# Performance work log

Measured on AMD Instinct MI355X. Metric: run time of the kernel, lower is better.

The kernel has to match this reference:

```python
import jax, jax.numpy as jnp
import numpy as np

N = 50000   # team_count (num nodes)
E = 800000  # num edges
D = 64      # embed_dim
C = 32      # conv_out_channels
K = 3       # Chebyshev order
B = 16384   # number of games (len(home))


def setup_inputs() -> dict:
    key = jax.random.key(0)
    ks = jax.random.split(key, 20)
    inp = {
        "edge_index": jax.random.randint(ks[0], (2, E), 0, N),
        "home": jax.random.randint(ks[1], (B,), 0, N),
        "away": jax.random.randint(ks[2], (B,), 0, N),
        "edge_weight": jax.random.uniform(ks[3], (E,), dtype=jnp.float32),
        "embedding": jax.random.normal(ks[4], (N, D), dtype=jnp.float32) * 0.1,
    }
    def W(k, i, o):
        return jax.random.normal(k, (K, i, o), dtype=jnp.float32) * 0.05
    inp["Wxz"] = W(ks[5], D, C); inp["Whz"] = W(ks[6], C, C)
    inp["Wxr"] = W(ks[7], D, C); inp["Whr"] = W(ks[8], C, C)
    inp["Wxh"] = W(ks[9], D, C); inp["Whh"] = W(ks[10], C, C)
    for i, name in enumerate(["bxz", "bhz", "bxr", "bhr", "bxh", "bhh"]):
        inp[name] = jax.random.normal(ks[11 + i], (C,), dtype=jnp.float32) * 0.01
    return inp


def _cheb(x, W, b, row, col, w_hat, n):
    """PyG ChebConv with sym normalization, lambda_max=2: L_hat = -D^-1/2 A D^-1/2."""
    def prop(t):  # L_hat @ t  via gather->scale->scatter over edges
        return jax.ops.segment_sum(w_hat[:, None] * t[row], col, num_segments=n)
    Tx0 = x
    out = Tx0 @ W[0]
    Tx1 = prop(Tx0)
    out = out + Tx1 @ W[1]
    for k in range(2, W.shape[0]):
        Tx2 = 2.0 * prop(Tx1) - Tx0
        out = out + Tx2 @ W[k]
        Tx0, Tx1 = Tx1, Tx2
    return out + b


def reference(edge_index, home, away, edge_weight, embedding,
              Wxz, Whz, Wxr, Whr, Wxh, Whh,
              bxz, bhz, bxr, bhr, bxh, bhh):
    row, col = edge_index[0], edge_index[1]
    n = embedding.shape[0]
    deg = jax.ops.segment_sum(edge_weight, row, num_segments=n)
    dinv = jnp.where(deg > 0, jax.lax.rsqrt(deg), 0.0)
    w_hat = -dinv[row] * edge_weight * dinv[col]

    x = embedding                       # [N, D]
    H = jnp.zeros((n, Wxz.shape[-1]), x.dtype)  # initial hidden state
    cheb = lambda t, W, b: _cheb(t, W, b, row, col, w_hat, n)

    Z = jax.nn.sigmoid(cheb(x, Wxz, bxz) + cheb(H, Whz, bhz))
    R = jax.nn.sigmoid(cheb(x, Wxr, bxr) + cheb(H, Whr, bhr))
    H_tilde = jnp.tanh(cheb(x, Wxh, bxh) + cheb(H * R, Whh, bhh))
    H = Z * H + (1.0 - Z) * H_tilde     # [N, C]

    h = jnp.concatenate([H[home], H[away]], axis=0)  # [2B, C]
    return jax.nn.softmax(h, axis=0)    # torch Softmax(dim=0)
```

## Files before the change

kernel.cpp:

```cpp
#include <hip/hip_runtime.h>
#include <hip/hip_fp16.h>
#include <math.h>

constexpr int N_   = 50000;
constexpr int E_   = 800000;
constexpr int D_   = 64;
constexpr int C_   = 32;
constexpr int B_   = 16384;
constexpr int TWOB = 2 * B_;
constexpr int NB_SM = 256;
constexpr int NBINS = (N_ + 255) / 256;
constexpr int EPB   = 4096;
constexpr int NCH   = (E_ + EPB - 1) / EPB;
constexpr int CAPBB = 64;
constexpr int CAPB  = 5120;
constexpr int GN  = 64;
constexpr int LDP = 68;
constexpr int NPAD = 50176;

__device__ inline float4 ld_h4(const ushort* p) {
    uint2 u = *reinterpret_cast<const uint2*>(p);
    __half2 h0 = *reinterpret_cast<__half2*>(&u.x);
    __half2 h1 = *reinterpret_cast<__half2*>(&u.y);
    float2 f0 = __half22float2(h0), f1 = __half22float2(h1);
    return make_float4(f0.x, f0.y, f1.x, f1.y);
}
__device__ inline void st_h4(ushort* p, float4 v) {
    __half2 h0 = __floats2half2_rn(v.x, v.y);
    __half2 h1 = __floats2half2_rn(v.z, v.w);
    uint2 u;
    u.x = *reinterpret_cast<unsigned*>(&h0);
    u.y = *reinterpret_cast<unsigned*>(&h1);
    *reinterpret_cast<uint2*>(p) = u;
}

__device__ inline void excl_scan256(int* sc, int t, int c0, int* st) {
    sc[t] = c0;
    __syncthreads();
#pragma unroll
    for (int off = 1; off < 256; off <<= 1) {
        int v = (t >= off) ? sc[t - off] : 0;
        __syncthreads();
        sc[t] += v;
        __syncthreads();
    }
    st[t] = sc[t] - c0;
}

__global__ __launch_bounds__(256) void k_bin(const int* __restrict__ row,
                                             const int* __restrict__ col,
                                             const float* __restrict__ ew,
                                             int* __restrict__ colCnt,
                                             int* __restrict__ rowCnt,
                                             int2* __restrict__ colBins2,
                                             int2* __restrict__ rowBins2) {
    __shared__ int cnt[256], st[256], cur[256], sc[256];
    __shared__ int2 buf[EPB];
    int t = threadIdx.x, blk = blockIdx.x;
    int base = blk * EPB;
    int nE = min(EPB, E_ - base);

    cnt[t] = 0;
    __syncthreads();
    for (int i = t; i < nE; i += 256) atomicAdd(&cnt[col[base + i] >> 8], 1);
    __syncthreads();
    int c0 = cnt[t];
    excl_scan256(sc, t, c0, st);
    cur[t] = 0;
    __syncthreads();
    for (int i = t; i < nE; i += 256) {
        int c = col[base + i], r = row[base + i];
        float w = ew[base + i];
        int p = st[c >> 8] + atomicAdd(&cur[c >> 8], 1);
        buf[p] = make_int2((c << 16) | r, __float_as_int(w));
    }
    __syncthreads();
    for (int i = t; i < nE; i += 256) {
        int2 e = buf[i];
        int bin = (int)(((unsigned)e.x) >> 24);
        int local = i - st[bin];
        if (local < CAPBB) colBins2[((size_t)bin * NCH + blk) * CAPBB + local] = e;
    }
    colCnt[blk * 256 + t] = min(c0, CAPBB);
    __syncthreads();

    cnt[t] = 0;
    __syncthreads();
    for (int i = t; i < nE; i += 256) atomicAdd(&cnt[row[base + i] >> 8], 1);
    __syncthreads();
    c0 = cnt[t];
    excl_scan256(sc, t, c0, st);
    cur[t] = 0;
    __syncthreads();
    for (int i = t; i < nE; i += 256) {
        int r = row[base + i];
        float w = ew[base + i];
        int p = st[r >> 8] + atomicAdd(&cur[r >> 8], 1);
        buf[p] = make_int2(r, __float_as_int(w));
    }
    __syncthreads();
    for (int i = t; i < nE; i += 256) {
        int2 e = buf[i];
        int bin = (int)(((unsigned)e.x) >> 8);
        int local = i - st[bin];
        if (local < CAPBB) rowBins2[((size_t)bin * NCH + blk) * CAPBB + local] = e;
    }
    rowCnt[blk * 256 + t] = min(c0, CAPBB);
}

__global__ __launch_bounds__(256) void k_deg(const int* __restrict__ rowCnt,
                                             const int2* __restrict__ rowBins2,
                                             float* __restrict__ dinv) {
    __shared__ float acc[256];
    int t = threadIdx.x, b = blockIdx.x;
    acc[t] = 0.f;
    __syncthreads();
    if (t < NCH) {
        int n = rowCnt[t * 256 + b];
        const int2* ch = rowBins2 + ((size_t)b * NCH + t) * CAPBB;
        for (int i = 0; i < n; ++i) {
            int2 e = ch[i];
            atomicAdd(&acc[e.x & 255], __int_as_float(e.y));
        }
    }
    __syncthreads();
    int r = b * 256 + t;
    if (r < N_) {
        float d = acc[t];
        dinv[r] = (d > 0.f) ? 1.f / sqrtf(d) : 0.f;
    }
}

__global__ __launch_bounds__(256) void k_sort(const int* __restrict__ colCnt,
                                              const int2* __restrict__ colBins2,
                                              const float* __restrict__ dinv,
                                              int2* __restrict__ edges,
                                              int2* __restrict__ percol,
                                              float* __restrict__ colsum) {
    __shared__ int cnt[256], st[256], cur[256], sc[256], pref[256];
    __shared__ int2 sbuf[CAPB];
    int t = threadIdx.x, b = blockIdx.x;
    if (b == 0 && t < 64) colsum[t] = 0.f;
    int myc = (t < NCH) ? colCnt[t * 256 + b] : 0;
    excl_scan256(sc, t, myc, pref);
    cnt[t] = 0;
    __syncthreads();
    if (t < NCH) {
        const int2* ch = colBins2 + ((size_t)b * NCH + t) * CAPBB;
        int p0 = pref[t];
        for (int i = 0; i < myc; ++i) {
            if (p0 + i < CAPB) {
                int2 e = ch[i];
                sbuf[p0 + i] = e;
                atomicAdd(&cnt[(((unsigned)e.x) >> 16) & 255], 1);
            }
        }
    }
    __syncthreads();
    int nb = min(sc[255], CAPB);
    int c0 = cnt[t];
    __syncthreads();
    excl_scan256(sc, t, c0, st);
    cur[t] = 0;
    __syncthreads();
    for (int i = t; i < nb; i += 256) {
        int2 e = sbuf[i];
        unsigned m = (unsigned)e.x;
        int r = (int)(m & 0xffffu);
        int c = (int)(m >> 16);
        float w = -__int_as_float(e.y) * dinv[r] * dinv[c];
        int clow = c & 255;
        int p = st[clow] + atomicAdd(&cur[clow], 1);
        edges[b * CAPB + p] = make_int2(r, __float_as_int(w));
    }
    percol[b * 256 + t] = make_int2(b * CAPB + st[t], cnt[t]);
}

__global__ __launch_bounds__(256) void k_prop1(const int2* __restrict__ percol,
                                               const int2* __restrict__ edges,
                                               const float* __restrict__ x,
                                               ushort* __restrict__ tx1h) {
    int node = (blockIdx.x * 256 + threadIdx.x) >> 6;
    if (node >= N_) return;
    int lane = threadIdx.x & 63;
    int eslot = lane >> 4;
    int f4 = (lane & 15) << 2;
    int2 oc = percol[node];
    int beg = oc.x, n = oc.y;
    float4 acc = {0.f, 0.f, 0.f, 0.f};
    for (int cb = 0; cb < n; cb += 16) {
        int2 er = edges[beg + cb + (lane & 15)];
        int   rr = er.x;
        float wr = __int_as_float(er.y);
#pragma unroll
        for (int k = 0; k < 4; ++k) {
            int idx = cb + 4 * k + eslot;
            int   r = __shfl(rr, 4 * k + eslot, 64);
            float w = __shfl(wr, 4 * k + eslot, 64);
            bool ok = idx < n;
            int  rs = ok ? r : 0;
            float wm = ok ? w : 0.f;
            float4 v = *reinterpret_cast<const float4*>(x + (size_t)rs * D_ + f4);
            acc.x += wm * v.x;
            acc.y += wm * v.y;
            acc.z += wm * v.z;
            acc.w += wm * v.w;
        }
    }
    acc.x += __shfl_xor(acc.x, 16, 64); acc.y += __shfl_xor(acc.y, 16, 64);
    acc.z += __shfl_xor(acc.z, 16, 64); acc.w += __shfl_xor(acc.w, 16, 64);
    acc.x += __shfl_xor(acc.x, 32, 64); acc.y += __shfl_xor(acc.y, 32, 64);
    acc.z += __shfl_xor(acc.z, 32, 64); acc.w += __shfl_xor(acc.w, 32, 64);
    if (eslot == 0) st_h4(tx1h + (size_t)node * D_ + f4, acc);
}

__global__ __launch_bounds__(256) void k_prop2(const int2* __restrict__ percol,
                                               const int2* __restrict__ edges,
                                               const ushort* __restrict__ tx1h,
                                               const float* __restrict__ x,
                                               ushort* __restrict__ tx2h) {
    int node = (blockIdx.x * 256 + threadIdx.x) >> 6;
    if (node >= N_) return;
    int lane = threadIdx.x & 63;
    int eslot = lane >> 4;
    int f4 = (lane & 15) << 2;
    int2 oc = percol[node];
    int beg = oc.x, n = oc.y;
    float4 acc = {0.f, 0.f, 0.f, 0.f};
    for (int cb = 0; cb < n; cb += 16) {
        int2 er = edges[beg + cb + (lane & 15)];
        int   rr = er.x;
        float wr = __int_as_float(er.y);
#pragma unroll
        for (int k = 0; k < 4; ++k) {
            int idx = cb + 4 * k + eslot;
            int   r = __shfl(rr, 4 * k + eslot, 64);
            float w = __shfl(wr, 4 * k + eslot, 64);
            bool ok = idx < n;
            int  rs = ok ? r : 0;
            float wm = ok ? w : 0.f;
            float4 v = ld_h4(tx1h + (size_t)rs * D_ + f4);
            acc.x += wm * v.x;
            acc.y += wm * v.y;
            acc.z += wm * v.z;
            acc.w += wm * v.w;
        }
    }
    acc.x += __shfl_xor(acc.x, 16, 64); acc.y += __shfl_xor(acc.y, 16, 64);
    acc.z += __shfl_xor(acc.z, 16, 64); acc.w += __shfl_xor(acc.w, 16, 64);
    acc.x += __shfl_xor(acc.x, 32, 64); acc.y += __shfl_xor(acc.y, 32, 64);
    acc.z += __shfl_xor(acc.z, 32, 64); acc.w += __shfl_xor(acc.w, 32, 64);
    if (eslot == 0) {
        float4 xv = *reinterpret_cast<const float4*>(x + (size_t)node * D_ + f4);
        float4 o = {2.f * acc.x - xv.x, 2.f * acc.y - xv.y,
                    2.f * acc.z - xv.z, 2.f * acc.w - xv.w};
        st_h4(tx2h + (size_t)node * D_ + f4, o);
    }
}

__global__ __launch_bounds__(256) void k_gates(const float* __restrict__ x,
                                               const ushort* __restrict__ tx1h,
                                               const ushort* __restrict__ tx2h,
                                               const float* __restrict__ Wxz,
                                               const float* __restrict__ Wxh,
                                               const float* __restrict__ bxz,
                                               const float* __restrict__ bhz,
                                               const float* __restrict__ bxh,
                                               const float* __restrict__ bhh,
                                               float* __restrict__ H) {
    __shared__ float lA[GN * LDP];
    __shared__ float lB[D_ * LDP];
    int t = threadIdx.x;
    int node0 = blockIdx.x * GN;
    int valid = min(GN, N_ - node0);
    int tn = t >> 4, tc = t & 15;
    float acc[4][4] = {};
    for (int ch = 0; ch < 3; ++ch) {
        if (ch == 0) {
            const float* s = x + (size_t)node0 * D_;
#pragma unroll
            for (int j = 0; j < 4; ++j) {
                int q = t * 4 + j * 1024;
                int nd = q >> 6, dd = q & 63;
                float4 v = {0.f, 0.f, 0.f, 0.f};
                if (nd < valid) v = *reinterpret_cast<const float4*>(s + q);
                *reinterpret_cast<float4*>(&lA[nd * LDP + dd]) = v;
            }
        } else {
            const ushort* s = ((ch == 1) ? tx1h : tx2h) + (size_t)node0 * D_;
#pragma unroll
            for (int j = 0; j < 4; ++j) {
                int q = t * 4 + j * 1024;
                int nd = q >> 6, dd = q & 63;
                float4 v = {0.f, 0.f, 0.f, 0.f};
                if (nd < valid) v = ld_h4(s + q);
                *reinterpret_cast<float4*>(&lA[nd * LDP + dd]) = v;
            }
        }
#pragma unroll
        for (int j = 0; j < 4; ++j) {
            int q = t * 4 + j * 1024;
            int dd = q >> 6, jj = q & 63;
            const float* wsrc = (jj < 32) ? (Wxz + ch * 2048 + dd * 32 + jj)
                                          : (Wxh + ch * 2048 + dd * 32 + (jj - 32));
            *reinterpret_cast<float4*>(&lB[dd * LDP + jj]) =
                *reinterpret_cast<const float4*>(wsrc);
        }
        __syncthreads();
#pragma unroll 4
        for (int k0 = 0; k0 < D_; k0 += 4) {
            float4 a[4], b[4];
#pragma unroll
            for (int i = 0; i < 4; ++i)
                a[i] = *reinterpret_cast<const float4*>(&lA[(tn * 4 + i) * LDP + k0]);
#pragma unroll
            for (int kk = 0; kk < 4; ++kk)
                b[kk] = *reinterpret_cast<const float4*>(&lB[(k0 + kk) * LDP + tc * 4]);
#pragma unroll
            for (int i = 0; i < 4; ++i) {
                acc[i][0] += a[i].x * b[0].x + a[i].y * b[1].x + a[i].z * b[2].x + a[i].w * b[3].x;
                acc[i][1] += a[i].x * b[0].y + a[i].y * b[1].y + a[i].z * b[2].y + a[i].w * b[3].y;
                acc[i][2] += a[i].x * b[0].z + a[i].y * b[1].z + a[i].z * b[2].z + a[i].w * b[3].z;
                acc[i][3] += a[i].x * b[0].w + a[i].y * b[1].w + a[i].z * b[2].w + a[i].w * b[3].w;
            }
        }
        __syncthreads();
    }
#pragma unroll
    for (int i = 0; i < 4; ++i) {
        float4 v = {acc[i][0], acc[i][1], acc[i][2], acc[i][3]};
        *reinterpret_cast<float4*>(&lA[(tn * 4 + i) * LDP + tc * 4]) = v;
    }
    __syncthreads();
#pragma unroll
    for (int m = 0; m < 8; ++m) {
        int idx = t + m * 256;
        int nd = idx >> 5, c = idx & 31;
        if (nd < valid) {
            float az = lA[nd * LDP + c]       + bxz[c] + bhz[c];
            float ah = lA[nd * LDP + 32 + c]  + bxh[c] + bhh[c];
            float z  = 1.f / (1.f + expf(-az));
            H[(size_t)(node0 + nd) * C_ + c] = (1.f - z) * tanhf(ah);
        }
    }
}

__global__ __launch_bounds__(256) void k_gexpsum2(const int* __restrict__ home,
                                                  const int* __restrict__ away,
                                                  const float* __restrict__ H,
                                                  float* __restrict__ hbuf,
                                                  float* __restrict__ colsum) {
    __shared__ float sm[8][32];
    int c = threadIdx.x & 31, g = threadIdx.x >> 5;
    float s = 0.f;
    for (int r0 = blockIdx.x * 8; r0 < TWOB; r0 += gridDim.x * 8) {
        int r = r0 + g;
        int node = (r < B_) ? home[r] : away[r - B_];
        float e = expf(H[(size_t)node * C_ + c]);
        hbuf[(size_t)r * C_ + c] = e;
        s += e;
    }
    sm[g][c] = s;
    __syncthreads();
    if (g < 4) sm[g][c] += sm[g + 4][c];
    __syncthreads();
    if (g < 2) sm[g][c] += sm[g + 2][c];
    __syncthreads();
    if (g == 0) atomicAdd(&colsum[c], sm[0][c] + sm[1][c]);
}

__global__ __launch_bounds__(256) void k_norm(const float* __restrict__ hbuf,
                                              const float* __restrict__ colsum,
                                              float* __restrict__ out) {
    int i = blockIdx.x * 256 + threadIdx.x;
    if (i < TWOB * C_ / 4) {
        float4 v = reinterpret_cast<const float4*>(hbuf)[i];
        int c0 = (i * 4) & 31;
        float4 s = *reinterpret_cast<const float4*>(colsum + c0);
        float4 o;
        o.x = v.x / s.x;
        o.y = v.y / s.y;
        o.z = v.z / s.z;
        o.w = v.w / s.w;
        reinterpret_cast<float4*>(out)[i] = o;
    }
}

extern "C" void kernel_launch(void* const* d_in, const int* in_sizes, int n_in,
                              void* d_out, int out_size, void* d_ws, size_t ws_size,
                              hipStream_t stream) {
    const int*   edge_index = (const int*)d_in[0];
    const int*   row  = edge_index;
    const int*   col  = edge_index + E_;
    const int*   home = (const int*)d_in[1];
    const int*   away = (const int*)d_in[2];
    const float* ew   = (const float*)d_in[3];
    const float* x    = (const float*)d_in[4];
    const float* Wxz  = (const float*)d_in[5];
    const float* Wxh  = (const float*)d_in[9];
    const float* bxz  = (const float*)d_in[11];
    const float* bhz  = (const float*)d_in[12];
    const float* bxh  = (const float*)d_in[15];
    const float* bhh  = (const float*)d_in[16];
    float* out = (float*)d_out;
    float* ws = (float*)d_ws;

    const size_t o_colCnt  = 0;
    const size_t o_rowCnt  = o_colCnt + (size_t)NCH * 256;
    const size_t o_colsum  = o_rowCnt + (size_t)NCH * 256;
    const size_t o_dinv    = o_colsum + 64;
    const size_t o_colBins2 = o_dinv + NPAD;
    const size_t o_rowBins2 = o_colBins2 + 2 * (size_t)NBINS * NCH * CAPBB;
    const size_t o_edges   = o_rowBins2 + 2 * (size_t)NBINS * NCH * CAPBB;
    const size_t o_percol  = o_edges + 2 * (size_t)NBINS * CAPB + 32;
    const size_t o_tx1h    = o_percol + 2 * (size_t)NBINS * 256;
    const size_t o_tx2h    = o_tx1h + (size_t)N_ * D_ / 2;
    const size_t o_H       = o_rowBins2;
    const size_t o_hbuf    = o_colBins2;

    int*    colCnt   = (int*)(ws + o_colCnt);
    int*    rowCnt   = (int*)(ws + o_rowCnt);
    int2*   colBins2 = (int2*)(ws + o_colBins2);
    int2*   rowBins2 = (int2*)(ws + o_rowBins2);
    int2*   edges    = (int2*)(ws + o_edges);
    int2*   percol   = (int2*)(ws + o_percol);
    ushort* tx1h     = (ushort*)(ws + o_tx1h);
    ushort* tx2h     = (ushort*)(ws + o_tx2h);

    k_bin <<<NCH, 256, 0, stream>>>(row, col, ew, colCnt, rowCnt, colBins2, rowBins2);
    k_deg <<<NBINS, 256, 0, stream>>>(rowCnt, rowBins2, ws + o_dinv);
    k_sort<<<NBINS, 256, 0, stream>>>(colCnt, colBins2, ws + o_dinv, edges, percol, ws + o_colsum);

    k_prop1<<<(N_ * 64 + 255) / 256, 256, 0, stream>>>(percol, edges, x, tx1h);
    k_prop2<<<(N_ * 64 + 255) / 256, 256, 0, stream>>>(percol, edges, tx1h, x, tx2h);

    k_gates<<<(N_ + GN - 1) / GN, 256, 0, stream>>>(x, tx1h, tx2h,
                                                    Wxz, Wxh, bxz, bhz, bxh, bhh, ws + o_H);

    k_gexpsum2<<<NB_SM, 256, 0, stream>>>(home, away, ws + o_H, ws + o_hbuf, ws + o_colsum);
    k_norm    <<<(TWOB * C_ / 4 + 255) / 256, 256, 0, stream>>>(ws + o_hbuf, ws + o_colsum, out);
}
```

Baseline: 145.4 us.

## Convert embedding to fp16 for gathers and parallelize bin reads across threads

The binning kernel now also converts the fp32 embedding into an fp16 copy, so the first propagation gathers half-width rows. The two prop kernels are merged into one template, and the second prop reads its subtraction term from the fp16 copy. k_deg and k_sort now read their chunk bins with 64 threads per chunk over 4 chunks at a time, replacing the old loop where one thread read a whole chunk serially. This cuts gather bandwidth and serial latency, but adds fp16 rounding error to the first Chebyshev term and extra conversion traffic.

```diff
diff --git a/kernel.cpp b/kernel.cpp
--- a/kernel.cpp
+++ b/kernel.cpp
@@ -50,6 +50,8 @@
 __global__ __launch_bounds__(256) void k_bin(const int* __restrict__ row,
                                              const int* __restrict__ col,
                                              const float* __restrict__ ew,
+                                             const float* __restrict__ x,
+                                             ushort* __restrict__ xh,
                                              int* __restrict__ colCnt,
                                              int* __restrict__ rowCnt,
                                              int2* __restrict__ colBins2,
@@ -106,20 +108,27 @@
         if (local < CAPBB) rowBins2[((size_t)bin * NCH + blk) * CAPBB + local] = e;
     }
     rowCnt[blk * 256 + t] = min(c0, CAPBB);
+
+    for (int i = blk * 256 + t; i < N_ * D_ / 4; i += NCH * 256) {
+        float4 v = reinterpret_cast<const float4*>(x)[i];
+        st_h4(xh + (size_t)i * 4, v);
+    }
 }
 
 __global__ __launch_bounds__(256) void k_deg(const int* __restrict__ rowCnt,
                                              const int2* __restrict__ rowBins2,
                                              float* __restrict__ dinv) {
     __shared__ float acc[256];
+    __shared__ int scnt[256];
     int t = threadIdx.x, b = blockIdx.x;
     acc[t] = 0.f;
-    __syncthreads();
-    if (t < NCH) {
-        int n = rowCnt[t * 256 + b];
-        const int2* ch = rowBins2 + ((size_t)b * NCH + t) * CAPBB;
-        for (int i = 0; i < n; ++i) {
-            int2 e = ch[i];
+    scnt[t] = (t < NCH) ? rowCnt[t * 256 + b] : 0;
+    __syncthreads();
+    int slot = t & 63;
+    for (int ch0 = 0; ch0 < NCH; ch0 += 4) {
+        int ch = ch0 + (t >> 6);
+        if (ch < NCH && slot < scnt[ch]) {
+            int2 e = rowBins2[((size_t)b * NCH + ch) * CAPBB + slot];
             atomicAdd(&acc[e.x & 255], __int_as_float(e.y));
         }
     }
@@ -137,21 +146,23 @@
                                               int2* __restrict__ edges,
                                               int2* __restrict__ percol,
                                               float* __restrict__ colsum) {
-    __shared__ int cnt[256], st[256], cur[256], sc[256], pref[256];
+    __shared__ int cnt[256], st[256], cur[256], sc[256], pref[256], chn[256];
     __shared__ int2 sbuf[CAPB];
     int t = threadIdx.x, b = blockIdx.x;
     if (b == 0 && t < 64) colsum[t] = 0.f;
     int myc = (t < NCH) ? colCnt[t * 256 + b] : 0;
+    chn[t] = myc;
     excl_scan256(sc, t, myc, pref);
     cnt[t] = 0;
     __syncthreads();
-    if (t < NCH) {
-        const int2* ch = colBins2 + ((size_t)b * NCH + t) * CAPBB;
-        int p0 = pref[t];
-        for (int i = 0; i < myc; ++i) {
-            if (p0 + i < CAPB) {
-                int2 e = ch[i];
-                sbuf[p0 + i] = e;
+    int slot = t & 63;
+    for (int ch0 = 0; ch0 < NCH; ch0 += 4) {
+        int ch = ch0 + (t >> 6);
+        if (ch < NCH && slot < chn[ch]) {
+            int2 e = colBins2[((size_t)b * NCH + ch) * CAPBB + slot];
+            int p = pref[ch] + slot;
+            if (p < CAPB) {
+                sbuf[p] = e;
                 atomicAdd(&cnt[(((unsigned)e.x) >> 16) & 255], 1);
             }
         }
@@ -176,10 +187,12 @@
     percol[b * 256 + t] = make_int2(b * CAPB + st[t], cnt[t]);
 }
 
-__global__ __launch_bounds__(256) void k_prop1(const int2* __restrict__ percol,
-                                               const int2* __restrict__ edges,
-                                               const float* __restrict__ x,
-                                               ushort* __restrict__ tx1h) {
+template <bool FUSE2>
+__global__ __launch_bounds__(256) void k_prop(const int2* __restrict__ percol,
+                                              const int2* __restrict__ edges,
+                                              const ushort* __restrict__ src,
+                                              const ushort* __restrict__ xsub,
+                                              ushort* __restrict__ dst) {
     int node = (blockIdx.x * 256 + threadIdx.x) >> 6;
     if (node >= N_) return;
     int lane = threadIdx.x & 63;
@@ -200,46 +213,7 @@
             bool ok = idx < n;
             int  rs = ok ? r : 0;
             float wm = ok ? w : 0.f;
-            float4 v = *reinterpret_cast<const float4*>(x + (size_t)rs * D_ + f4);
-            acc.x += wm * v.x;
-            acc.y += wm * v.y;
-            acc.z += wm * v.z;
-            acc.w += wm * v.w;
-        }
-    }
-    acc.x += __shfl_xor(acc.x, 16, 64); acc.y += __shfl_xor(acc.y, 16, 64);
-    acc.z += __shfl_xor(acc.z, 16, 64); acc.w += __shfl_xor(acc.w, 16, 64);
-    acc.x += __shfl_xor(acc.x, 32, 64); acc.y += __shfl_xor(acc.y, 32, 64);
-    acc.z += __shfl_xor(acc.z, 32, 64); acc.w += __shfl_xor(acc.w, 32, 64);
-    if (eslot == 0) st_h4(tx1h + (size_t)node * D_ + f4, acc);
-}
-
-__global__ __launch_bounds__(256) void k_prop2(const int2* __restrict__ percol,
-                                               const int2* __restrict__ edges,
-                                               const ushort* __restrict__ tx1h,
-                                               const float* __restrict__ x,
-                                               ushort* __restrict__ tx2h) {
-    int node = (blockIdx.x * 256 + threadIdx.x) >> 6;
-    if (node >= N_) return;
-    int lane = threadIdx.x & 63;
-    int eslot = lane >> 4;
-    int f4 = (lane & 15) << 2;
-    int2 oc = percol[node];
-    int beg = oc.x, n = oc.y;
-    float4 acc = {0.f, 0.f, 0.f, 0.f};
-    for (int cb = 0; cb < n; cb += 16) {
-        int2 er = edges[beg + cb + (lane & 15)];
-        int   rr = er.x;
-        float wr = __int_as_float(er.y);
-#pragma unroll
-        for (int k = 0; k < 4; ++k) {
-            int idx = cb + 4 * k + eslot;
-            int   r = __shfl(rr, 4 * k + eslot, 64);
-            float w = __shfl(wr, 4 * k + eslot, 64);
-            bool ok = idx < n;
-            int  rs = ok ? r : 0;
-            float wm = ok ? w : 0.f;
-            float4 v = ld_h4(tx1h + (size_t)rs * D_ + f4);
+            float4 v = ld_h4(src + (size_t)rs * D_ + f4);
             acc.x += wm * v.x;
             acc.y += wm * v.y;
             acc.z += wm * v.z;
@@ -251,10 +225,15 @@
     acc.x += __shfl_xor(acc.x, 32, 64); acc.y += __shfl_xor(acc.y, 32, 64);
     acc.z += __shfl_xor(acc.z, 32, 64); acc.w += __shfl_xor(acc.w, 32, 64);
     if (eslot == 0) {
-        float4 xv = *reinterpret_cast<const float4*>(x + (size_t)node * D_ + f4);
-        float4 o = {2.f * acc.x - xv.x, 2.f * acc.y - xv.y,
-                    2.f * acc.z - xv.z, 2.f * acc.w - xv.w};
-        st_h4(tx2h + (size_t)node * D_ + f4, o);
+        float4 o = acc;
+        if (FUSE2) {
+            float4 xv = ld_h4(xsub + (size_t)node * D_ + f4);
+            o.x = 2.f * acc.x - xv.x;
+            o.y = 2.f * acc.y - xv.y;
+            o.z = 2.f * acc.z - xv.z;
+            o.w = 2.f * acc.w - xv.w;
+        }
+        st_h4(dst + (size_t)node * D_ + f4, o);
     }
 }
 
@@ -413,7 +392,8 @@
     const size_t o_rowBins2 = o_colBins2 + 2 * (size_t)NBINS * NCH * CAPBB;
     const size_t o_edges   = o_rowBins2 + 2 * (size_t)NBINS * NCH * CAPBB;
     const size_t o_percol  = o_edges + 2 * (size_t)NBINS * CAPB + 32;
-    const size_t o_tx1h    = o_percol + 2 * (size_t)NBINS * 256;
+    const size_t o_xh      = o_percol + 2 * (size_t)NBINS * 256;
+    const size_t o_tx1h    = o_xh + (size_t)N_ * D_ / 2;
     const size_t o_tx2h    = o_tx1h + (size_t)N_ * D_ / 2;
     const size_t o_H       = o_rowBins2;
     const size_t o_hbuf    = o_colBins2;
@@ -424,15 +404,16 @@
     int2*   rowBins2 = (int2*)(ws + o_rowBins2);
     int2*   edges    = (int2*)(ws + o_edges);
     int2*   percol   = (int2*)(ws + o_percol);
+    ushort* xh       = (ushort*)(ws + o_xh);
     ushort* tx1h     = (ushort*)(ws + o_tx1h);
     ushort* tx2h     = (ushort*)(ws + o_tx2h);
 
-    k_bin <<<NCH, 256, 0, stream>>>(row, col, ew, colCnt, rowCnt, colBins2, rowBins2);
+    k_bin <<<NCH, 256, 0, stream>>>(row, col, ew, x, xh, colCnt, rowCnt, colBins2, rowBins2);
     k_deg <<<NBINS, 256, 0, stream>>>(rowCnt, rowBins2, ws + o_dinv);
     k_sort<<<NBINS, 256, 0, stream>>>(colCnt, colBins2, ws + o_dinv, edges, percol, ws + o_colsum);
 
-    k_prop1<<<(N_ * 64 + 255) / 256, 256, 0, stream>>>(percol, edges, x, tx1h);
-    k_prop2<<<(N_ * 64 + 255) / 256, 256, 0, stream>>>(percol, edges, tx1h, x, tx2h);
+    k_prop<false><<<(N_ * 64 + 255) / 256, 256, 0, stream>>>(percol, edges, xh, nullptr, tx1h);
+    k_prop<true> <<<(N_ * 64 + 255) / 256, 256, 0, stream>>>(percol, edges, tx1h, xh, tx2h);
 
     k_gates<<<(N_ + GN - 1) / GN, 256, 0, stream>>>(x, tx1h, tx2h,
                                                     Wxz, Wxh, bxz, bhz, bxh, bhh, ws + o_H);
```

Result: slower. 167.7 us (+15.3%).

## Fuse softmax exp-sum and normalize into one kernel with grid barrier

Applied to the files above, without the earlier changes.

Merges the exp/column-sum kernel and the normalization kernel into a single launch. Each of the 256 blocks keeps its 128 rows of exp values in registers, then waits at a software grid barrier (atomic counter spin) before dividing by the column sums and writing the output. This removes a kernel launch and the round trip of the intermediate exp buffer through global memory. It relies on all 256 blocks being co-resident, and it adds a spin-wait plus a done counter that is reset in k_sort.

```diff
diff --git a/kernel.cpp b/kernel.cpp
--- a/kernel.cpp
+++ b/kernel.cpp
@@ -136,11 +136,11 @@
                                               const float* __restrict__ dinv,
                                               int2* __restrict__ edges,
                                               int2* __restrict__ percol,
-                                              float* __restrict__ colsum) {
+                                              float* __restrict__ colsum_flag) {
     __shared__ int cnt[256], st[256], cur[256], sc[256], pref[256];
     __shared__ int2 sbuf[CAPB];
     int t = threadIdx.x, b = blockIdx.x;
-    if (b == 0 && t < 64) colsum[t] = 0.f;
+    if (b == 0 && t < 96) colsum_flag[t] = 0.f;
     int myc = (t < NCH) ? colCnt[t * 256 + b] : 0;
     excl_scan256(sc, t, myc, pref);
     cnt[t] = 0;
@@ -345,20 +345,23 @@
     }
 }
 
-__global__ __launch_bounds__(256) void k_gexpsum2(const int* __restrict__ home,
-                                                  const int* __restrict__ away,
-                                                  const float* __restrict__ H,
-                                                  float* __restrict__ hbuf,
-                                                  float* __restrict__ colsum) {
+__global__ __launch_bounds__(256) void k_expnorm(const int* __restrict__ home,
+                                                 const int* __restrict__ away,
+                                                 const float* __restrict__ H,
+                                                 float* __restrict__ colsum,
+                                                 int* __restrict__ done,
+                                                 float* __restrict__ out) {
     __shared__ float sm[8][32];
     int c = threadIdx.x & 31, g = threadIdx.x >> 5;
+    int base = blockIdx.x * (TWOB / NB_SM);
+    float e[16];
     float s = 0.f;
-    for (int r0 = blockIdx.x * 8; r0 < TWOB; r0 += gridDim.x * 8) {
-        int r = r0 + g;
+#pragma unroll
+    for (int i = 0; i < 16; ++i) {
+        int r = base + i * 8 + g;
         int node = (r < B_) ? home[r] : away[r - B_];
-        float e = expf(H[(size_t)node * C_ + c]);
-        hbuf[(size_t)r * C_ + c] = e;
-        s += e;
+        e[i] = expf(H[(size_t)node * C_ + c]);
+        s += e[i];
     }
     sm[g][c] = s;
     __syncthreads();
@@ -367,22 +370,18 @@
     if (g < 2) sm[g][c] += sm[g + 2][c];
     __syncthreads();
     if (g == 0) atomicAdd(&colsum[c], sm[0][c] + sm[1][c]);
-}
-
-__global__ __launch_bounds__(256) void k_norm(const float* __restrict__ hbuf,
-                                              const float* __restrict__ colsum,
-                                              float* __restrict__ out) {
-    int i = blockIdx.x * 256 + threadIdx.x;
-    if (i < TWOB * C_ / 4) {
-        float4 v = reinterpret_cast<const float4*>(hbuf)[i];
-        int c0 = (i * 4) & 31;
-        float4 s = *reinterpret_cast<const float4*>(colsum + c0);
-        float4 o;
-        o.x = v.x / s.x;
-        o.y = v.y / s.y;
-        o.z = v.z / s.z;
-        o.w = v.w / s.w;
-        reinterpret_cast<float4*>(out)[i] = o;
+    __syncthreads();
+    if (threadIdx.x == 0) {
+        __threadfence();
+        atomicAdd(done, 1);
+        while (atomicAdd(done, 0) < NB_SM) { }
+    }
+    __syncthreads();
+    float inv = 1.f / atomicAdd(&colsum[c], 0.f);
+#pragma unroll
+    for (int i = 0; i < 16; ++i) {
+        int r = base + i * 8 + g;
+        out[(size_t)r * C_ + c] = e[i] * inv;
     }
 }
 
@@ -408,7 +407,8 @@
     const size_t o_colCnt  = 0;
     const size_t o_rowCnt  = o_colCnt + (size_t)NCH * 256;
     const size_t o_colsum  = o_rowCnt + (size_t)NCH * 256;
-    const size_t o_dinv    = o_colsum + 64;
+    const size_t o_done    = o_colsum + 64;
+    const size_t o_dinv    = o_colsum + 96;
     const size_t o_colBins2 = o_dinv + NPAD;
     const size_t o_rowBins2 = o_colBins2 + 2 * (size_t)NBINS * NCH * CAPBB;
     const size_t o_edges   = o_rowBins2 + 2 * (size_t)NBINS * NCH * CAPBB;
@@ -416,7 +416,6 @@
     const size_t o_tx1h    = o_percol + 2 * (size_t)NBINS * 256;
     const size_t o_tx2h    = o_tx1h + (size_t)N_ * D_ / 2;
     const size_t o_H       = o_rowBins2;
-    const size_t o_hbuf    = o_colBins2;
 
     int*    colCnt   = (int*)(ws + o_colCnt);
     int*    rowCnt   = (int*)(ws + o_rowCnt);
@@ -437,6 +436,6 @@
     k_gates<<<(N_ + GN - 1) / GN, 256, 0, stream>>>(x, tx1h, tx2h,
                                                     Wxz, Wxh, bxz, bhz, bxh, bhh, ws + o_H);
 
-    k_gexpsum2<<<NB_SM, 256, 0, stream>>>(home, away, ws + o_H, ws + o_hbuf, ws + o_colsum);
-    k_norm    <<<(TWOB * C_ / 4 + 255) / 256, 256, 0, stream>>>(ws + o_hbuf, ws + o_colsum, out);
-}
+    k_expnorm<<<NB_SM, 256, 0, stream>>>(home, away, ws + o_H, ws + o_colsum,
+                                         (int*)(ws + o_done), out);
+}
```

Measured after the change: 210.4 us. 1.45x slower.

## Fold row-side degree scaling into prescaled fp16 features and fuse degree with sort

Applied to the files above, without the earlier changes.

The symmetric normalisation is refactored. The row factor dinv[r] is moved into a prescaled fp16 copy of x, and into tx1, which is stored as dinv*tx1 and rescaled by sqrt(deg) in the gate GEMM. Edge weights now only need the local column's dinv, so the degree and sort kernels merge into one launch with no global dinv lookup. Prop1 also gathers half-precision rows instead of fp32, halving gather traffic, at the cost of an extra prescaled buffer write and some fp16 rounding of x.

```diff
diff --git a/kernel.cpp b/kernel.cpp
--- a/kernel.cpp
+++ b/kernel.cpp
@@ -108,39 +108,59 @@
     rowCnt[blk * 256 + t] = min(c0, CAPBB);
 }
 
-__global__ __launch_bounds__(256) void k_deg(const int* __restrict__ rowCnt,
-                                             const int2* __restrict__ rowBins2,
-                                             float* __restrict__ dinv) {
-    __shared__ float acc[256];
+__global__ __launch_bounds__(256) void k_degsort(const int* __restrict__ rowCnt,
+                                                 const int2* __restrict__ rowBins2,
+                                                 const int* __restrict__ colCnt,
+                                                 const int2* __restrict__ colBins2,
+                                                 const float* __restrict__ x,
+                                                 ushort* __restrict__ xph,
+                                                 float* __restrict__ dinv,
+                                                 float* __restrict__ sdeg,
+                                                 int2* __restrict__ edges,
+                                                 int2* __restrict__ percol,
+                                                 float* __restrict__ colsum) {
+    __shared__ float dacc[256], sd[256];
+    __shared__ int cnt[256], st[256], cur[256], sc[256], pref[256];
+    __shared__ int2 sbuf[CAPB];
     int t = threadIdx.x, b = blockIdx.x;
-    acc[t] = 0.f;
+    if (b == 0 && t < 64) colsum[t] = 0.f;
+
+    dacc[t] = 0.f;
     __syncthreads();
     if (t < NCH) {
         int n = rowCnt[t * 256 + b];
         const int2* ch = rowBins2 + ((size_t)b * NCH + t) * CAPBB;
         for (int i = 0; i < n; ++i) {
             int2 e = ch[i];
-            atomicAdd(&acc[e.x & 255], __int_as_float(e.y));
-        }
-    }
-    __syncthreads();
-    int r = b * 256 + t;
-    if (r < N_) {
-        float d = acc[t];
-        dinv[r] = (d > 0.f) ? 1.f / sqrtf(d) : 0.f;
-    }
-}
-
-__global__ __launch_bounds__(256) void k_sort(const int* __restrict__ colCnt,
-                                              const int2* __restrict__ colBins2,
-                                              const float* __restrict__ dinv,
-                                              int2* __restrict__ edges,
-                                              int2* __restrict__ percol,
-                                              float* __restrict__ colsum) {
-    __shared__ int cnt[256], st[256], cur[256], sc[256], pref[256];
-    __shared__ int2 sbuf[CAPB];
-    int t = threadIdx.x, b = blockIdx.x;
-    if (b == 0 && t < 64) colsum[t] = 0.f;
+            atomicAdd(&dacc[e.x & 255], __int_as_float(e.y));
+        }
+    }
+    __syncthreads();
+    {
+        float d = dacc[t];
+        float di = (d > 0.f) ? 1.f / sqrtf(d) : 0.f;
+        sd[t] = di;
+        int node = b * 256 + t;
+        if (node < N_) {
+            dinv[node] = di;
+            sdeg[node] = (d > 0.f) ? sqrtf(d) : 0.f;
+        }
+    }
+    __syncthreads();
+
+#pragma unroll
+    for (int j = 0; j < 16; ++j) {
+        int idx = j * 256 + t;
+        int nl = idx >> 4;
+        int node = b * 256 + nl;
+        if (node < N_) {
+            const float4 v = *reinterpret_cast<const float4*>(x + (size_t)node * D_ + (idx & 15) * 4);
+            float s = sd[nl];
+            float4 o = {v.x * s, v.y * s, v.z * s, v.w * s};
+            st_h4(xph + (size_t)node * D_ + (idx & 15) * 4, o);
+        }
+    }
+
     int myc = (t < NCH) ? colCnt[t * 256 + b] : 0;
     excl_scan256(sc, t, myc, pref);
     cnt[t] = 0;
@@ -167,9 +187,8 @@
         int2 e = sbuf[i];
         unsigned m = (unsigned)e.x;
         int r = (int)(m & 0xffffu);
-        int c = (int)(m >> 16);
-        float w = -__int_as_float(e.y) * dinv[r] * dinv[c];
-        int clow = c & 255;
+        int clow = (int)(m >> 16) & 255;
+        float w = -__int_as_float(e.y) * sd[clow];
         int p = st[clow] + atomicAdd(&cur[clow], 1);
         edges[b * CAPB + p] = make_int2(r, __float_as_int(w));
     }
@@ -178,8 +197,9 @@
 
 __global__ __launch_bounds__(256) void k_prop1(const int2* __restrict__ percol,
                                                const int2* __restrict__ edges,
-                                               const float* __restrict__ x,
-                                               ushort* __restrict__ tx1h) {
+                                               const ushort* __restrict__ xph,
+                                               const float* __restrict__ dinv,
+                                               ushort* __restrict__ tx1s) {
     int node = (blockIdx.x * 256 + threadIdx.x) >> 6;
     if (node >= N_) return;
     int lane = threadIdx.x & 63;
@@ -200,7 +220,7 @@
             bool ok = idx < n;
             int  rs = ok ? r : 0;
             float wm = ok ? w : 0.f;
-            float4 v = *reinterpret_cast<const float4*>(x + (size_t)rs * D_ + f4);
+            float4 v = ld_h4(xph + (size_t)rs * D_ + f4);
             acc.x += wm * v.x;
             acc.y += wm * v.y;
             acc.z += wm * v.z;
@@ -211,12 +231,16 @@
     acc.z += __shfl_xor(acc.z, 16, 64); acc.w += __shfl_xor(acc.w, 16, 64);
     acc.x += __shfl_xor(acc.x, 32, 64); acc.y += __shfl_xor(acc.y, 32, 64);
     acc.z += __shfl_xor(acc.z, 32, 64); acc.w += __shfl_xor(acc.w, 32, 64);
-    if (eslot == 0) st_h4(tx1h + (size_t)node * D_ + f4, acc);
+    if (eslot == 0) {
+        float di = dinv[node];
+        float4 o = {di * acc.x, di * acc.y, di * acc.z, di * acc.w};
+        st_h4(tx1s + (size_t)node * D_ + f4, o);
+    }
 }
 
 __global__ __launch_bounds__(256) void k_prop2(const int2* __restrict__ percol,
                                                const int2* __restrict__ edges,
-                                               const ushort* __restrict__ tx1h,
+                                               const ushort* __restrict__ tx1s,
                                                const float* __restrict__ x,
                                                ushort* __restrict__ tx2h) {
     int node = (blockIdx.x * 256 + threadIdx.x) >> 6;
@@ -239,7 +263,7 @@
             bool ok = idx < n;
             int  rs = ok ? r : 0;
             float wm = ok ? w : 0.f;
-            float4 v = ld_h4(tx1h + (size_t)rs * D_ + f4);
+            float4 v = ld_h4(tx1s + (size_t)rs * D_ + f4);
             acc.x += wm * v.x;
             acc.y += wm * v.y;
             acc.z += wm * v.z;
@@ -259,8 +283,9 @@
 }
 
 __global__ __launch_bounds__(256) void k_gates(const float* __restrict__ x,
-                                               const ushort* __restrict__ tx1h,
+                                               const ushort* __restrict__ tx1s,
                                                const ushort* __restrict__ tx2h,
+                                               const float* __restrict__ sdeg,
                                                const float* __restrict__ Wxz,
                                                const float* __restrict__ Wxh,
                                                const float* __restrict__ bxz,
@@ -286,8 +311,22 @@
                 if (nd < valid) v = *reinterpret_cast<const float4*>(s + q);
                 *reinterpret_cast<float4*>(&lA[nd * LDP + dd]) = v;
             }
+        } else if (ch == 1) {
+            const ushort* s = tx1s + (size_t)node0 * D_;
+#pragma unroll
+            for (int j = 0; j < 4; ++j) {
+                int q = t * 4 + j * 1024;
+                int nd = q >> 6, dd = q & 63;
+                float4 v = {0.f, 0.f, 0.f, 0.f};
+                if (nd < valid) {
+                    v = ld_h4(s + q);
+                    float sg = sdeg[node0 + nd];
+                    v.x *= sg; v.y *= sg; v.z *= sg; v.w *= sg;
+                }
+                *reinterpret_cast<float4*>(&lA[nd * LDP + dd]) = v;
+            }
         } else {
-            const ushort* s = ((ch == 1) ? tx1h : tx2h) + (size_t)node0 * D_;
+            const ushort* s = tx2h + (size_t)node0 * D_;
 #pragma unroll
             for (int j = 0; j < 4; ++j) {
                 int q = t * 4 + j * 1024;
@@ -409,12 +448,14 @@
     const size_t o_rowCnt  = o_colCnt + (size_t)NCH * 256;
     const size_t o_colsum  = o_rowCnt + (size_t)NCH * 256;
     const size_t o_dinv    = o_colsum + 64;
-    const size_t o_colBins2 = o_dinv + NPAD;
+    const size_t o_sdeg    = o_dinv + NPAD;
+    const size_t o_colBins2 = o_sdeg + NPAD;
     const size_t o_rowBins2 = o_colBins2 + 2 * (size_t)NBINS * NCH * CAPBB;
     const size_t o_edges   = o_rowBins2 + 2 * (size_t)NBINS * NCH * CAPBB;
     const size_t o_percol  = o_edges + 2 * (size_t)NBINS * CAPB + 32;
-    const size_t o_tx1h    = o_percol + 2 * (size_t)NBINS * 256;
-    const size_t o_tx2h    = o_tx1h + (size_t)N_ * D_ / 2;
+    const size_t o_xph     = o_percol + 2 * (size_t)NBINS * 256;
+    const size_t o_tx1s    = o_xph + (size_t)N_ * D_ / 2;
+    const size_t o_tx2h    = o_tx1s + (size_t)N_ * D_ / 2;
     const size_t o_H       = o_rowBins2;
     const size_t o_hbuf    = o_colBins2;
 
@@ -424,17 +465,18 @@
     int2*   rowBins2 = (int2*)(ws + o_rowBins2);
     int2*   edges    = (int2*)(ws + o_edges);
     int2*   percol   = (int2*)(ws + o_percol);
-    ushort* tx1h     = (ushort*)(ws + o_tx1h);
+    ushort* xph      = (ushort*)(ws + o_xph);
+    ushort* tx1s     = (ushort*)(ws + o_tx1s);
     ushort* tx2h     = (ushort*)(ws + o_tx2h);
 
-    k_bin <<<NCH, 256, 0, stream>>>(row, col, ew, colCnt, rowCnt, colBins2, rowBins2);
-    k_deg <<<NBINS, 256, 0, stream>>>(rowCnt, rowBins2, ws + o_dinv);
-    k_sort<<<NBINS, 256, 0, stream>>>(colCnt, colBins2, ws + o_dinv, edges, percol, ws + o_colsum);
-
-    k_prop1<<<(N_ * 64 + 255) / 256, 256, 0, stream>>>(percol, edges, x, tx1h);
-    k_prop2<<<(N_ * 64 + 255) / 256, 256, 0, stream>>>(percol, edges, tx1h, x, tx2h);
-
-    k_gates<<<(N_ + GN - 1) / GN, 256, 0, stream>>>(x, tx1h, tx2h,
+    k_bin    <<<NCH, 256, 0, stream>>>(row, col, ew, colCnt, rowCnt, colBins2, rowBins2);
+    k_degsort<<<NBINS, 256, 0, stream>>>(rowCnt, rowBins2, colCnt, colBins2, x, xph,
+                                         ws + o_dinv, ws + o_sdeg, edges, percol, ws + o_colsum);
+
+    k_prop1<<<(N_ * 64 + 255) / 256, 256, 0, stream>>>(percol, edges, xph, ws + o_dinv, tx1s);
+    k_prop2<<<(N_ * 64 + 255) / 256, 256, 0, stream>>>(percol, edges, tx1s, x, tx2h);
+
+    k_gates<<<(N_ + GN - 1) / GN, 256, 0, stream>>>(x, tx1s, tx2h, ws + o_sdeg,
                                                     Wxz, Wxh, bxz, bhz, bxh, bhh, ws + o_H);
 
     k_gexpsum2<<<NB_SM, 256, 0, stream>>>(home, away, ws + o_H, ws + o_hbuf, ws + o_colsum);
```

After: 144.4 us (median of 2 runs). No clear change (-0.7%).
